# Optimization experiments

Measured on AMD Instinct MI355X. Metric: run time of the kernel, lower is better.

The kernel has to match this reference:

```python
import math
import jax, jax.numpy as jnp
import numpy as np

D_MODEL, N_HEADS, D_HEAD, D_INNER = 512, 8, 64, 2048
QLEN, MLEN, BATCH = 2048, 2048, 2


def _layernorm(x, g, b, eps=1e-5):
    mu = jnp.mean(x, axis=-1, keepdims=True)
    var = jnp.var(x, axis=-1, keepdims=True)
    return (x - mu) * jax.lax.rsqrt(var + eps) * g + b


def _rel_shift(x):
    # x: [qlen, klen, B, n] -> Transformer-XL relative shift
    q, k, b, n = x.shape
    x = jnp.pad(x, ((0, 0), (1, 0), (0, 0), (0, 0)))  # zero-pad key dim at front
    x = x.reshape(k + 1, q, b, n)[1:].reshape(q, k, b, n)
    return x


def setup_inputs() -> dict:
    key = jax.random.key(0)
    ks = jax.random.split(key, 16)
    nd = N_HEADS * D_HEAD
    s = 0.02
    return {
        "x": jax.random.normal(ks[0], (QLEN, BATCH, D_MODEL), jnp.float32),
        "r": jax.random.normal(ks[1], (QLEN + MLEN, D_MODEL), jnp.float32),
        "u": jax.random.normal(ks[2], (N_HEADS, D_HEAD), jnp.float32) * s,
        "v": jax.random.normal(ks[3], (N_HEADS, D_HEAD), jnp.float32) * s,
        "mems": jax.random.normal(ks[4], (MLEN, BATCH, D_MODEL), jnp.float32),
        "Wqkv": jax.random.normal(ks[5], (3 * nd, D_MODEL), jnp.float32) * s,
        "Wr": jax.random.normal(ks[6], (nd, D_MODEL), jnp.float32) * s,
        "Wo": jax.random.normal(ks[7], (D_MODEL, nd), jnp.float32) * s,
        "ln1_g": jnp.ones((D_MODEL,), jnp.float32),
        "ln1_b": jnp.zeros((D_MODEL,), jnp.float32),
        "W1": jax.random.normal(ks[8], (D_MODEL, D_INNER), jnp.float32) * s,
        "b1": jnp.zeros((D_INNER,), jnp.float32),
        "W2": jax.random.normal(ks[9], (D_INNER, D_MODEL), jnp.float32) * s,
        "b2": jnp.zeros((D_MODEL,), jnp.float32),
        "ln2_g": jnp.ones((D_MODEL,), jnp.float32),
        "ln2_b": jnp.zeros((D_MODEL,), jnp.float32),
    }


def reference(x, r, u, v, mems, Wqkv, Wr, Wo, ln1_g, ln1_b, W1, b1, W2, b2, ln2_g, ln2_b):
    qlen, B, d_model = x.shape
    n_heads, d_head = u.shape
    cat = jnp.concatenate([mems, x], axis=0)          # [klen, B, d_model]
    klen = cat.shape[0]
    mlen = klen - qlen

    qkv = cat @ Wqkv.T                                 # [klen, B, 3*n*d]
    q, k, val = jnp.split(qkv, 3, axis=-1)
    q = q[-qlen:].reshape(qlen, B, n_heads, d_head)
    k = k.reshape(klen, B, n_heads, d_head)
    val = val.reshape(klen, B, n_heads, d_head)
    rk = (r @ Wr.T).reshape(klen, n_heads, d_head)     # relative key heads

    AC = jnp.einsum('ibnd,jbnd->ijbn', q + u, k)       # content score
    BD = _rel_shift(jnp.einsum('ibnd,jnd->ijbn', q + v, rk))  # position score
    score = (AC + BD) * (1.0 / math.sqrt(d_head))      # [qlen, klen, B, n]

    # causal mask with memory: query i attends keys j <= i + mlen
    mask = jnp.arange(klen)[None, :] > (jnp.arange(qlen)[:, None] + mlen)
    score = jnp.where(mask[:, :, None, None], jnp.float32(-1e30), score)
    attn = jax.nn.softmax(score, axis=1)

    out = jnp.einsum('ijbn,jbnd->ibnd', attn, val).reshape(qlen, B, n_heads * d_head)
    out = out @ Wo.T
    h = _layernorm(x + out, ln1_g, ln1_b)              # post-LN attention

    core = jax.nn.relu(h @ W1 + b1) @ W2 + b2          # PositionwiseFF
    return _layernorm(h + core, ln2_g, ln2_b)
```

## Files before the change

### kernel.cpp

```cpp
#include <hip/hip_runtime.h>
#include <hip/hip_bf16.h>

#define QLEN 2048
#define MLEN 2048
#define KLEN 4096
#define BATCH 2
#define DMODEL 512
#define NHEADS 8
#define DHEAD 64
#define DINNER 2048

typedef __attribute__((ext_vector_type(8))) short  vs8;
typedef __attribute__((ext_vector_type(8))) __bf16 vbf8;
typedef __attribute__((ext_vector_type(4))) float  vf4;

__device__ __forceinline__ float bf2f(ushort h) {
    union { unsigned u; float f; } c; c.u = ((unsigned)h) << 16; return c.f;
}
__device__ __forceinline__ ushort f2bf(float f) {
    return __builtin_bit_cast(unsigned short, (__bf16)f);
}
__device__ __forceinline__ vf4 mfma16(vs8 a, vs8 b, vf4 c) {
    return __builtin_amdgcn_mfma_f32_16x16x32_bf16(
        __builtin_bit_cast(vbf8, a), __builtin_bit_cast(vbf8, b), c, 0, 0, 0);
}
__device__ __forceinline__ void gl16(const ushort* g, ushort* l) {
    __builtin_amdgcn_global_load_lds(
        (const __attribute__((address_space(1))) void*)g,
        (__attribute__((address_space(3))) void*)l, 16, 0, 0);
}
#define WAITV4 asm volatile("s_waitcnt vmcnt(4)" ::: "memory")
#define WAITV0 asm volatile("s_waitcnt vmcnt(0)" ::: "memory")
__device__ __forceinline__ void barx() {
    asm volatile("" ::: "memory");
    __builtin_amdgcn_s_barrier();
    asm volatile("" ::: "memory");
}

__global__ void cvt_bf(const float* __restrict__ in, ushort* __restrict__ out, int nel4) {
    int i = blockIdx.x * 256 + threadIdx.x;
    if (i < nel4) {
        float4 f = ((const float4*)in)[i];
        ushort4 o; o.x = f2bf(f.x); o.y = f2bf(f.y); o.z = f2bf(f.z); o.w = f2bf(f.w);
        ((ushort4*)out)[i] = o;
    }
}

__global__ void cvt_cat(const float* __restrict__ mems, const float* __restrict__ x,
                        ushort* __restrict__ out) {
    int i = blockIdx.x * 256 + threadIdx.x;
    const int half4 = MLEN * BATCH * DMODEL / 4;
    if (i < 2 * half4) {
        float4 f = (i < half4) ? ((const float4*)mems)[i] : ((const float4*)x)[i - half4];
        ushort4 o; o.x = f2bf(f.x); o.y = f2bf(f.y); o.z = f2bf(f.z); o.w = f2bf(f.w);
        ((ushort4*)out)[i] = o;
    }
}

__global__ void cvt_tr(const float* __restrict__ in, ushort* __restrict__ out, int R, int C) {
    __shared__ float t[32][33];
    const int c0 = blockIdx.x * 32, r0 = blockIdx.y * 32;
    const int tx = threadIdx.x & 31, ty = threadIdx.x >> 5;
#pragma unroll
    for (int q = 0; q < 4; ++q) {
        int r = ty + q * 8;
        t[r][tx] = in[(size_t)(r0 + r) * C + c0 + tx];
    }
    __syncthreads();
#pragma unroll
    for (int q = 0; q < 4; ++q) {
        int c = ty + q * 8;
        out[(size_t)(c0 + c) * R + r0 + tx] = f2bf(t[tx][c]);
    }
}

__global__ void vtrans(const ushort* __restrict__ qkv, ushort* __restrict__ vT) {
    __shared__ __align__(16) ushort t_lds[64][72];
    const int j0 = blockIdx.x * 64, n = blockIdx.y, b = blockIdx.z;
    const int tid = threadIdx.x;
#pragma unroll
    for (int p = 0; p < 2; ++p) {
        int u2 = p * 256 + tid;
        int j = u2 >> 3, d8 = (u2 & 7) * 8;
        vs8 v8 = *(const vs8*)(qkv + ((size_t)(j0 + j) * BATCH + b) * 1536 + 1024 + n * 64 + d8);
#pragma unroll
        for (int e = 0; e < 8; ++e) t_lds[d8 + e][j] = (ushort)v8[e];
    }
    __syncthreads();
#pragma unroll
    for (int p = 0; p < 2; ++p) {
        int u2 = p * 256 + tid;
        int d = u2 >> 3, j8 = (u2 & 7) * 8;
        vs8 o8 = *(const vs8*)&t_lds[d][j8];
        *(vs8*)(vT + ((size_t)(b * NHEADS + n) * 64 + d) * KLEN + j0 + j8) = o8;
    }
}

template <int EPI>
__global__ __launch_bounds__(256)
void gemm_bt(const ushort* __restrict__ A, const ushort* __restrict__ B,
             void* __restrict__ C0, void* __restrict__ C1,
             const float* __restrict__ bias, int M, int N, int K, int kc, int ldc) {
    __shared__ __align__(16) ushort As[2][128 * 32];
    __shared__ __align__(16) ushort Bs[2][128 * 32];
    const int n0 = blockIdx.x * 128;
    const int m0 = blockIdx.y * 128;
    const int kb = blockIdx.z * kc;
    void* C = blockIdx.z ? C1 : C0;
    const int tid = threadIdx.x;
    const int lane = tid & 63, wave = tid >> 6;
    const int wr = wave >> 1, wc = wave & 1;
    const int lr = lane & 15, lg = lane >> 4;
    vf4 acc[4][4] = {};

    auto stage = [&](int bi, int k0) {
#pragma unroll
        for (int t = 0; t < 2; ++t) {
            int u = t * 256 + tid;
            int row = u >> 2, cu = u & 3;
            int sc = cu ^ ((row >> 1) & 3);
            gl16(&A[(size_t)(m0 + row) * K + k0 + sc * 8],
                 &As[bi][t * 2048 + (tid & 192) * 8]);
            gl16(&B[(size_t)(n0 + row) * K + k0 + sc * 8],
                 &Bs[bi][t * 2048 + (tid & 192) * 8]);
        }
    };

    const int nt = kc >> 5;
    stage(0, kb);
    int cur = 0;
    for (int t = 0; t < nt; ++t) {
        if (t + 1 < nt) { stage(cur ^ 1, kb + (t + 1) * 32); WAITV4; }
        else { WAITV0; }
        barx();
        vs8 af[4], bfr[4];
#pragma unroll
        for (int m = 0; m < 4; ++m) {
            int rr = wr * 64 + m * 16 + lr;
            af[m] = *(const vs8*)&As[cur][rr * 32 + (lg ^ ((rr >> 1) & 3)) * 8];
        }
#pragma unroll
        for (int nn = 0; nn < 4; ++nn) {
            int rr = wc * 64 + nn * 16 + lr;
            bfr[nn] = *(const vs8*)&Bs[cur][rr * 32 + (lg ^ ((rr >> 1) & 3)) * 8];
        }
#pragma unroll
        for (int m = 0; m < 4; ++m)
#pragma unroll
            for (int nn = 0; nn < 4; ++nn)
                acc[m][nn] = mfma16(af[m], bfr[nn], acc[m][nn]);
        barx();
        cur ^= 1;
    }

#pragma unroll
    for (int m = 0; m < 4; ++m) {
#pragma unroll
        for (int nn = 0; nn < 4; ++nn) {
            int row0 = m0 + wr * 64 + m * 16 + lg * 4;
            int col  = n0 + wc * 64 + nn * 16 + lr;
#pragma unroll
            for (int rr = 0; rr < 4; ++rr) {
                float vv = acc[m][nn][rr];
                size_t off = (size_t)(row0 + rr) * ldc + col;
                if (EPI == 0) ((float*)C)[off] = vv;
                else if (EPI == 1) ((ushort*)C)[off] = f2bf(vv);
                else if (EPI == 2) {
                    float t2 = vv + bias[col];
                    ((ushort*)C)[off] = f2bf(t2 > 0.f ? t2 : 0.f);
                } else {
                    ((ushort*)C)[(((size_t)(col >> 6)) << 18) + (size_t)(row0 + rr) * 64 + (col & 63)]
                        = f2bf(vv);
                }
            }
        }
    }
}

__global__ __launch_bounds__(256, 3)
void attn2(const ushort* __restrict__ qkv, const ushort* __restrict__ rkh,
           const ushort* __restrict__ vT, const float* __restrict__ uu,
           const float* __restrict__ vv, float* __restrict__ part_l,
           float* __restrict__ part_o) {
    __shared__ __align__(16) ushort K_lds[64 * 64];
    __shared__ __align__(16) ushort V_lds[64 * 64];
    __shared__ __align__(16) ushort w_lds[4][16 * 84];
    __shared__ __align__(16) ushort p_lds[4][16 * 72];

    const int chunk = blockIdx.x & 3, qb = 31 - (blockIdx.x >> 2);
    const int b = blockIdx.y, n = blockIdx.z;
    const int tid = threadIdx.x, lane = tid & 63, w = tid >> 6;
    const int lr = lane & 15, lg = lane >> 4;
    const int i0w = qb * 64 + w * 16;

    ushort* wl = w_lds[w];
    ushort* pl = p_lds[w];
    const ushort* rh  = rkh + ((size_t)n << 18);
    const ushort* vTh = vT + (size_t)(b * NHEADS + n) * 64 * KLEN;

    const float S = 0.18033688011112042f;
    vs8 aqu[2], aqv[2];
#pragma unroll
    for (int kk = 0; kk < 2; ++kk) {
        int d0 = kk * 32 + lg * 8;
        vs8 q8 = *(const vs8*)(qkv + ((size_t)(i0w + lr + MLEN) * BATCH + b) * 1536 + n * 64 + d0);
#pragma unroll
        for (int e = 0; e < 8; ++e) {
            float qf = bf2f((ushort)q8[e]);
            aqu[kk][e] = (short)f2bf((qf + uu[n * 64 + d0 + e]) * S);
            aqv[kk][e] = (short)f2bf((qf + vv[n * 64 + d0 + e]) * S);
        }
    }

    const vf4 zero4 = {0.f, 0.f, 0.f, 0.f};
    vf4 o[4] = {zero4, zero4, zero4, zero4};
    float l_run[4] = {0.f, 0.f, 0.f, 0.f};

    const int jstart = chunk * 1024;
    int avail = qb * 64 + 2111 - jstart;
    int niter = avail < 0 ? 0 : (avail >> 6) + 1;
    niter = niter > 16 ? 16 : niter;

    const int slot = lane & 7;
    vs8 kreg[2], vreg[2];
    auto ldkv = [&](int j0) {
#pragma unroll
        for (int p2 = 0; p2 < 2; ++p2) {
            int row = p2 * 32 + w * 8 + (lane >> 3);
            int g = (slot - row) & 7;
            kreg[p2] = *(const vs8*)(qkv + ((size_t)(j0 + row) * BATCH + b) * 1536 + 512 + n * 64 + g * 8);
            vreg[p2] = *(const vs8*)(vTh + (size_t)row * KLEN + j0 + g * 8);
        }
    };
    auto wrkv = [&]() {
#pragma unroll
        for (int p2 = 0; p2 < 2; ++p2) {
            int row = p2 * 32 + w * 8 + (lane >> 3);
            *(vs8*)&K_lds[row * 64 + slot * 8] = kreg[p2];
            *(vs8*)&V_lds[row * 64 + slot * 8] = vreg[p2];
        }
    };

    if (niter > 0) {
        ldkv(jstart);
        wrkv();
        __syncthreads();
        for (int it = 0; it < niter; ++it) {
            const int j0 = jstart + it * 64;
            const bool more = (it + 1 < niter);
            if (more) ldkv(j0 + 64);

            vf4 acc_s[4] = {zero4, zero4, zero4, zero4};
#pragma unroll
            for (int q = 0; q < 4; ++q) {
                int jr = q * 16 + lr;
#pragma unroll
                for (int kk = 0; kk < 2; ++kk) {
                    vs8 kb = *(const vs8*)&K_lds[jr * 64 + ((kk * 4 + lg + jr) & 7) * 8];
                    acc_s[q] = mfma16(aqu[kk], kb, acc_s[q]);
                }
            }
            const int mbase = j0 - i0w + 2032;
#pragma unroll
            for (int wg = 0; wg < 5; ++wg) {
                vf4 aw = zero4;
                int mrow = mbase + wg * 16 + lr;
                mrow = mrow > KLEN - 1 ? KLEN - 1 : mrow;
#pragma unroll
                for (int kk = 0; kk < 2; ++kk) {
                    vs8 rb = *(const vs8*)(rh + (size_t)mrow * 64 + kk * 32 + lg * 8);
                    aw = mfma16(aqv[kk], rb, aw);
                }
#pragma unroll
                for (int r = 0; r < 4; ++r)
                    wl[(lg * 4 + r) * 84 + wg * 16 + lr] = f2bf(aw[r]);
            }

            const int thr = qb * 64 + w * 16 + 2048 - j0;
            if (thr >= 63) {
#pragma unroll
                for (int r = 0; r < 4; ++r) {
                    int il = lg * 4 + r;
                    float psum = 0.f;
#pragma unroll
                    for (int q = 0; q < 4; ++q) {
                        int jl = q * 16 + lr;
                        float p4 = __builtin_amdgcn_exp2f(
                            acc_s[q][r] + bf2f(wl[il * 84 + jl - il + 15]));
                        psum += p4;
                        pl[il * 72 + jl] = f2bf(p4);
                    }
#pragma unroll
                    for (int off = 1; off < 16; off <<= 1) psum += __shfl_xor(psum, off);
                    l_run[r] += psum;
                }
            } else {
#pragma unroll
                for (int r = 0; r < 4; ++r) {
                    int il = lg * 4 + r;
                    float psum = 0.f;
#pragma unroll
                    for (int q = 0; q < 4; ++q) {
                        int jl = q * 16 + lr;
                        float s = acc_s[q][r] + bf2f(wl[il * 84 + jl - il + 15]);
                        if (jl - il > thr) s = -1e30f;
                        float p4 = __builtin_amdgcn_exp2f(s);
                        psum += p4;
                        pl[il * 72 + jl] = f2bf(p4);
                    }
#pragma unroll
                    for (int off = 1; off < 16; off <<= 1) psum += __shfl_xor(psum, off);
                    l_run[r] += psum;
                }
            }

#pragma unroll
            for (int jk = 0; jk < 2; ++jk) {
                vs8 pf = *(const vs8*)&pl[lr * 72 + jk * 32 + lg * 8];
#pragma unroll
                for (int dg = 0; dg < 4; ++dg) {
                    int dr = dg * 16 + lr;
                    vs8 vfr = *(const vs8*)&V_lds[dr * 64 + ((jk * 4 + lg + dr) & 7) * 8];
                    o[dg] = mfma16(pf, vfr, o[dg]);
                }
            }
            __syncthreads();
            if (more) { wrkv(); __syncthreads(); }
        }
    }

#pragma unroll
    for (int r = 0; r < 4; ++r) {
        int i = i0w + lg * 4 + r;
        int pr = (i * 2 + b) * 8 + n;
        size_t base = ((size_t)chunk * 32768 + pr) * 64;
#pragma unroll
        for (int dg = 0; dg < 4; ++dg)
            part_o[base + dg * 16 + lr] = o[dg][r];
        if (lr == 0) part_l[chunk * 32768 + pr] = l_run[r];
    }
}

__global__ __launch_bounds__(256)
void combine(const float* __restrict__ part_l, const float* __restrict__ part_o,
             ushort* __restrict__ ao) {
    int t = blockIdx.x * 256 + threadIdx.x;
    int pr = t >> 4, d4 = (t & 15) * 4;
    float l = 0.f;
    float4 s = {0.f, 0.f, 0.f, 0.f};
#pragma unroll
    for (int c = 0; c < 4; ++c) {
        l += part_l[c * 32768 + pr];
        float4 a = *(const float4*)&part_o[((size_t)c * 32768 + pr) * 64 + d4];
        s.x += a.x; s.y += a.y; s.z += a.z; s.w += a.w;
    }
    float rl = 1.f / l;
    int i2b = pr >> 3, n = pr & 7;
    ushort* dst = ao + (size_t)i2b * 512 + n * 64 + d4;
    dst[0] = f2bf(s.x * rl);
    dst[1] = f2bf(s.y * rl);
    dst[2] = f2bf(s.z * rl);
    dst[3] = f2bf(s.w * rl);
}

__global__ __launch_bounds__(256)
void ln_fuse(const float* __restrict__ base, const float* __restrict__ pa,
             const float* __restrict__ pb, const float* __restrict__ bias,
             const float* __restrict__ g, const float* __restrict__ bb,
             float* __restrict__ of32, ushort* __restrict__ obf) {
    const int row = blockIdx.x * 4 + (threadIdx.x >> 6);
    const int lane = threadIdx.x & 63;
    const size_t off0 = (size_t)row * DMODEL + lane * 8;
    float vals[8];
    float s = 0.f, s2 = 0.f;
#pragma unroll
    for (int e = 0; e < 8; ++e) {
        float t = base[off0 + e] + pa[off0 + e];
        if (pb) t += pb[off0 + e];
        if (bias) t += bias[lane * 8 + e];
        vals[e] = t; s += t; s2 += t * t;
    }
#pragma unroll
    for (int o = 1; o < 64; o <<= 1) { s += __shfl_xor(s, o); s2 += __shfl_xor(s2, o); }
    const float mean = s * (1.f / DMODEL);
    const float var = s2 * (1.f / DMODEL) - mean * mean;
    const float rstd = rsqrtf(var + 1e-5f);
#pragma unroll
    for (int e = 0; e < 8; ++e) {
        int c = lane * 8 + e;
        float y = (vals[e] - mean) * rstd * g[c] + bb[c];
        if (of32) of32[(size_t)row * DMODEL + c] = y;
        if (obf)  obf[(size_t)row * DMODEL + c] = f2bf(y);
    }
}

extern "C" void kernel_launch(void* const* d_in, const int* in_sizes, int n_in,
                              void* d_out, int out_size, void* d_ws, size_t ws_size,
                              hipStream_t stream) {
    const float* x    = (const float*)d_in[0];
    const float* r    = (const float*)d_in[1];
    const float* u    = (const float*)d_in[2];
    const float* v    = (const float*)d_in[3];
    const float* mems = (const float*)d_in[4];
    const float* Wqkv = (const float*)d_in[5];
    const float* Wr   = (const float*)d_in[6];
    const float* Wo   = (const float*)d_in[7];
    const float* ln1g = (const float*)d_in[8];
    const float* ln1b = (const float*)d_in[9];
    const float* W1   = (const float*)d_in[10];
    const float* b1   = (const float*)d_in[11];
    const float* W2   = (const float*)d_in[12];
    const float* b2   = (const float*)d_in[13];
    const float* ln2g = (const float*)d_in[14];
    const float* ln2b = (const float*)d_in[15];
    float* out = (float*)d_out;

    char* p = (char*)d_ws;
    auto alloc = [&](size_t bytes) { char* q = p; p += (bytes + 255) & ~(size_t)255; return q; };
    const size_t MB84 = (size_t)QLEN * BATCH * 512 * 4;
    ushort* cat_bf  = (ushort*)alloc((size_t)KLEN * BATCH * DMODEL * 2);
    ushort* wqkv_bf = (ushort*)alloc((size_t)1536 * 512 * 2);
    ushort* r_bf    = (ushort*)alloc((size_t)KLEN * 512 * 2);
    ushort* wr_bf   = (ushort*)alloc((size_t)512 * 512 * 2);
    ushort* wo_bf   = (ushort*)alloc((size_t)512 * 512 * 2);
    ushort* w1t_bf  = (ushort*)alloc((size_t)DINNER * 512 * 2);
    ushort* w2t_bf  = (ushort*)alloc((size_t)512 * DINNER * 2);
    ushort* qkv_bf  = (ushort*)alloc((size_t)KLEN * BATCH * 1536 * 2);
    ushort* rkh_bf  = (ushort*)alloc((size_t)KLEN * 512 * 2);
    ushort* vT      = (ushort*)alloc((size_t)BATCH * NHEADS * 64 * KLEN * 2);
    ushort* ao_bf   = (ushort*)alloc((size_t)QLEN * BATCH * 512 * 2);
    ushort* h_bf    = (ushort*)alloc((size_t)QLEN * BATCH * 512 * 2);
    float*  part_l  = (float*)alloc((size_t)4 * 32768 * 4);
    char*   big     = alloc(5 * MB84);
    float*  part_o  = (float*)big;
    float*  proj1a  = (float*)big;
    float*  proj1b  = (float*)(big + MB84);
    float*  h_f32   = (float*)(big + 2 * MB84);
    ushort* ff1_bf  = (ushort*)(big + 3 * MB84);
    float*  proj2a  = proj1a;
    float*  proj2b  = proj1b;

    const int MROWS = QLEN * BATCH;
    const int CATROWS = KLEN * BATCH;

    cvt_cat<<<(CATROWS * DMODEL / 4 + 255) / 256, 256, 0, stream>>>(mems, x, cat_bf);
    cvt_bf<<<(KLEN * 512 / 4 + 255) / 256, 256, 0, stream>>>(r, r_bf, KLEN * 512 / 4);
    cvt_bf<<<(1536 * 512 / 4 + 255) / 256, 256, 0, stream>>>(Wqkv, wqkv_bf, 1536 * 512 / 4);
    cvt_bf<<<(512 * 512 / 4 + 255) / 256, 256, 0, stream>>>(Wr, wr_bf, 512 * 512 / 4);
    cvt_bf<<<(512 * 512 / 4 + 255) / 256, 256, 0, stream>>>(Wo, wo_bf, 512 * 512 / 4);
    cvt_tr<<<dim3(DINNER / 32, 512 / 32), 256, 0, stream>>>(W1, w1t_bf, 512, DINNER);
    cvt_tr<<<dim3(512 / 32, DINNER / 32), 256, 0, stream>>>(W2, w2t_bf, DINNER, 512);

    gemm_bt<1><<<dim3(1024 / 128, CATROWS / 128, 1), 256, 0, stream>>>(
        cat_bf, wqkv_bf + (size_t)512 * 512, qkv_bf + 512, nullptr, nullptr,
        CATROWS, 1024, 512, 512, 1536);
    gemm_bt<1><<<dim3(512 / 128, 4096 / 128, 1), 256, 0, stream>>>(
        cat_bf + (size_t)4096 * 512, wqkv_bf, qkv_bf + (size_t)4096 * 1536, nullptr, nullptr,
        4096, 512, 512, 512, 1536);
    gemm_bt<3><<<dim3(512 / 128, KLEN / 128, 1), 256, 0, stream>>>(
        r_bf, wr_bf, rkh_bf, nullptr, nullptr, KLEN, 512, 512, 512, 512);

    vtrans<<<dim3(KLEN / 64, NHEADS, BATCH), 256, 0, stream>>>(qkv_bf, vT);
    attn2<<<dim3(128, BATCH, NHEADS), 256, 0, stream>>>(qkv_bf, rkh_bf, vT, u, v, part_l, part_o);
    combine<<<32768 * 16 / 256, 256, 0, stream>>>(part_l, part_o, ao_bf);

    gemm_bt<0><<<dim3(512 / 128, MROWS / 128, 2), 256, 0, stream>>>(
        ao_bf, wo_bf, proj1a, proj1b, nullptr, MROWS, 512, 512, 256, 512);
    ln_fuse<<<MROWS / 4, 256, 0, stream>>>(x, proj1a, proj1b, nullptr, ln1g, ln1b, h_f32, h_bf);

    gemm_bt<2><<<dim3(DINNER / 128, MROWS / 128, 1), 256, 0, stream>>>(
        h_bf, w1t_bf, ff1_bf, nullptr, b1, MROWS, DINNER, 512, 512, 2048);
    gemm_bt<0><<<dim3(512 / 128, MROWS / 128, 2), 256, 0, stream>>>(
        ff1_bf, w2t_bf, proj2a, proj2b, nullptr, MROWS, 512, 2048, 1024, 512);
    ln_fuse<<<MROWS / 4, 256, 0, stream>>>(h_f32, proj2a, proj2b, b2, ln2g, ln2b, out, nullptr);
}
```

Measured before the change: 356.5 us.

## Transpose attention MFMAs to keep P in registers, halve key-split chunks

The attention kernel now computes scores transposed (K as the A operand), so the probability tile stays in registers. It is packed to bf16 and redistributed with lane shuffles instead of being staged through per-wave LDS. The key range is split into 2 chunks instead of 4, and the partial outputs are written as bf16 via a coalesced LDS staging step. This shrinks the combine pass and the partial-result traffic. Occupancy hint rises to 5 waves per SIMD, at the cost of fewer blocks, longer per-block loops and bf16 rounding of the partial sums.

```diff
diff --git a/kernel.cpp b/kernel.cpp
--- a/kernel.cpp
+++ b/kernel.cpp
@@ -19,6 +19,11 @@
 }
 __device__ __forceinline__ ushort f2bf(float f) {
     return __builtin_bit_cast(unsigned short, (__bf16)f);
+}
+__device__ __forceinline__ unsigned cvtpk(float lo, float hi) {
+    unsigned r;
+    asm("v_cvt_pk_bf16_f32 %0, %1, %2" : "=v"(r) : "v"(lo), "v"(hi));
+    return r;
 }
 __device__ __forceinline__ vf4 mfma16(vs8 a, vs8 b, vf4 c) {
     return __builtin_amdgcn_mfma_f32_16x16x32_bf16(
@@ -177,24 +182,22 @@
     }
 }
 
-__global__ __launch_bounds__(256, 3)
+__global__ __launch_bounds__(256, 5)
 void attn2(const ushort* __restrict__ qkv, const ushort* __restrict__ rkh,
            const ushort* __restrict__ vT, const float* __restrict__ uu,
            const float* __restrict__ vv, float* __restrict__ part_l,
-           float* __restrict__ part_o) {
+           ushort* __restrict__ part_o) {
     __shared__ __align__(16) ushort K_lds[64 * 64];
     __shared__ __align__(16) ushort V_lds[64 * 64];
     __shared__ __align__(16) ushort w_lds[4][16 * 84];
-    __shared__ __align__(16) ushort p_lds[4][16 * 72];
-
-    const int chunk = blockIdx.x & 3, qb = 31 - (blockIdx.x >> 2);
+
+    const int chunk = blockIdx.x & 1, qb = 31 - (blockIdx.x >> 1);
     const int b = blockIdx.y, n = blockIdx.z;
     const int tid = threadIdx.x, lane = tid & 63, w = tid >> 6;
     const int lr = lane & 15, lg = lane >> 4;
     const int i0w = qb * 64 + w * 16;
 
     ushort* wl = w_lds[w];
-    ushort* pl = p_lds[w];
     const ushort* rh  = rkh + ((size_t)n << 18);
     const ushort* vTh = vT + (size_t)(b * NHEADS + n) * 64 * KLEN;
 
@@ -214,12 +217,12 @@
 
     const vf4 zero4 = {0.f, 0.f, 0.f, 0.f};
     vf4 o[4] = {zero4, zero4, zero4, zero4};
-    float l_run[4] = {0.f, 0.f, 0.f, 0.f};
-
-    const int jstart = chunk * 1024;
+    float l_run = 0.f;
+
+    const int jstart = chunk * 2048;
     int avail = qb * 64 + 2111 - jstart;
     int niter = avail < 0 ? 0 : (avail >> 6) + 1;
-    niter = niter > 16 ? 16 : niter;
+    niter = niter > 32 ? 32 : niter;
 
     const int slot = lane & 7;
     vs8 kreg[2], vreg[2];
@@ -241,126 +244,128 @@
         }
     };
 
-    if (niter > 0) {
-        ldkv(jstart);
-        wrkv();
+    ldkv(jstart);
+    wrkv();
+    __syncthreads();
+    for (int it = 0; it < niter; ++it) {
+        const int j0 = jstart + it * 64;
+        const bool more = (it + 1 < niter);
+        if (more) ldkv(j0 + 64);
+
+        vf4 acc_s[4] = {zero4, zero4, zero4, zero4};
+#pragma unroll
+        for (int jg = 0; jg < 4; ++jg) {
+            int jr = jg * 16 + lr;
+#pragma unroll
+            for (int kk = 0; kk < 2; ++kk) {
+                vs8 kb = *(const vs8*)&K_lds[jr * 64 + ((kk * 4 + lg + jr) & 7) * 8];
+                acc_s[jg] = mfma16(kb, aqu[kk], acc_s[jg]);
+            }
+        }
+        const int mbase = j0 - i0w + 2032;
+#pragma unroll
+        for (int wg = 0; wg < 5; ++wg) {
+            vf4 aw = zero4;
+            int mrow = mbase + wg * 16 + lr;
+            mrow = mrow > KLEN - 1 ? KLEN - 1 : mrow;
+#pragma unroll
+            for (int kk = 0; kk < 2; ++kk) {
+                vs8 rb = *(const vs8*)(rh + (size_t)mrow * 64 + kk * 32 + lg * 8);
+                aw = mfma16(rb, aqv[kk], aw);
+            }
+#pragma unroll
+            for (int r = 0; r < 4; ++r)
+                wl[lr * 84 + wg * 16 + lg * 4 + r] = f2bf(aw[r]);
+        }
+
+        const int thr = i0w + 2048 - j0;
+        const int bw = lr * 83 + 15;
+        if (thr >= 63) {
+#pragma unroll
+            for (int jg = 0; jg < 4; ++jg)
+#pragma unroll
+                for (int r = 0; r < 4; ++r) {
+                    float p4 = __builtin_amdgcn_exp2f(
+                        acc_s[jg][r] + bf2f(wl[bw + jg * 16 + lg * 4 + r]));
+                    acc_s[jg][r] = p4;
+                    l_run += p4;
+                }
+        } else {
+#pragma unroll
+            for (int jg = 0; jg < 4; ++jg)
+#pragma unroll
+                for (int r = 0; r < 4; ++r) {
+                    int jrel = jg * 16 + lg * 4 + r;
+                    float p4 = (jrel - lr > thr) ? 0.f
+                        : __builtin_amdgcn_exp2f(
+                              acc_s[jg][r] + bf2f(wl[bw + jg * 16 + lg * 4 + r]));
+                    acc_s[jg][r] = p4;
+                    l_run += p4;
+                }
+        }
+
+        unsigned pw0[4], pw1[4];
+#pragma unroll
+        for (int jg = 0; jg < 4; ++jg) {
+            pw0[jg] = cvtpk(acc_s[jg][0], acc_s[jg][1]);
+            pw1[jg] = cvtpk(acc_s[jg][2], acc_s[jg][3]);
+        }
+
+        const int srcA = (lg & 1) * 32 + lr, srcB = srcA + 16;
+        const bool hi = (lg >> 1) != 0;
+#pragma unroll
+        for (int kk = 0; kk < 2; ++kk) {
+            unsigned a0 = __shfl(pw0[2 * kk], srcA), b0 = __shfl(pw0[2 * kk + 1], srcA);
+            unsigned a1 = __shfl(pw1[2 * kk], srcA), b1 = __shfl(pw1[2 * kk + 1], srcA);
+            unsigned a2 = __shfl(pw0[2 * kk], srcB), b2 = __shfl(pw0[2 * kk + 1], srcB);
+            unsigned a3 = __shfl(pw1[2 * kk], srcB), b3 = __shfl(pw1[2 * kk + 1], srcB);
+            int4 pu = { (int)(hi ? b0 : a0), (int)(hi ? b1 : a1),
+                        (int)(hi ? b2 : a2), (int)(hi ? b3 : a3) };
+            vs8 pfrag = __builtin_bit_cast(vs8, pu);
+#pragma unroll
+            for (int dg = 0; dg < 4; ++dg) {
+                int dr = dg * 16 + lr;
+                vs8 vfr = *(const vs8*)&V_lds[dr * 64 + ((kk * 4 + lg + dr) & 7) * 8];
+                o[dg] = mfma16(vfr, pfrag, o[dg]);
+            }
+        }
         __syncthreads();
-        for (int it = 0; it < niter; ++it) {
-            const int j0 = jstart + it * 64;
-            const bool more = (it + 1 < niter);
-            if (more) ldkv(j0 + 64);
-
-            vf4 acc_s[4] = {zero4, zero4, zero4, zero4};
-#pragma unroll
-            for (int q = 0; q < 4; ++q) {
-                int jr = q * 16 + lr;
-#pragma unroll
-                for (int kk = 0; kk < 2; ++kk) {
-                    vs8 kb = *(const vs8*)&K_lds[jr * 64 + ((kk * 4 + lg + jr) & 7) * 8];
-                    acc_s[q] = mfma16(aqu[kk], kb, acc_s[q]);
-                }
-            }
-            const int mbase = j0 - i0w + 2032;
-#pragma unroll
-            for (int wg = 0; wg < 5; ++wg) {
-                vf4 aw = zero4;
-                int mrow = mbase + wg * 16 + lr;
-                mrow = mrow > KLEN - 1 ? KLEN - 1 : mrow;
-#pragma unroll
-                for (int kk = 0; kk < 2; ++kk) {
-                    vs8 rb = *(const vs8*)(rh + (size_t)mrow * 64 + kk * 32 + lg * 8);
-                    aw = mfma16(aqv[kk], rb, aw);
-                }
-#pragma unroll
-                for (int r = 0; r < 4; ++r)
-                    wl[(lg * 4 + r) * 84 + wg * 16 + lr] = f2bf(aw[r]);
-            }
-
-            const int thr = qb * 64 + w * 16 + 2048 - j0;
-            if (thr >= 63) {
-#pragma unroll
-                for (int r = 0; r < 4; ++r) {
-                    int il = lg * 4 + r;
-                    float psum = 0.f;
-#pragma unroll
-                    for (int q = 0; q < 4; ++q) {
-                        int jl = q * 16 + lr;
-                        float p4 = __builtin_amdgcn_exp2f(
-                            acc_s[q][r] + bf2f(wl[il * 84 + jl - il + 15]));
-                        psum += p4;
-                        pl[il * 72 + jl] = f2bf(p4);
-                    }
-#pragma unroll
-                    for (int off = 1; off < 16; off <<= 1) psum += __shfl_xor(psum, off);
-                    l_run[r] += psum;
-                }
-            } else {
-#pragma unroll
-                for (int r = 0; r < 4; ++r) {
-                    int il = lg * 4 + r;
-                    float psum = 0.f;
-#pragma unroll
-                    for (int q = 0; q < 4; ++q) {
-                        int jl = q * 16 + lr;
-                        float s = acc_s[q][r] + bf2f(wl[il * 84 + jl - il + 15]);
-                        if (jl - il > thr) s = -1e30f;
-                        float p4 = __builtin_amdgcn_exp2f(s);
-                        psum += p4;
-                        pl[il * 72 + jl] = f2bf(p4);
-                    }
-#pragma unroll
-                    for (int off = 1; off < 16; off <<= 1) psum += __shfl_xor(psum, off);
-                    l_run[r] += psum;
-                }
-            }
-
-#pragma unroll
-            for (int jk = 0; jk < 2; ++jk) {
-                vs8 pf = *(const vs8*)&pl[lr * 72 + jk * 32 + lg * 8];
-#pragma unroll
-                for (int dg = 0; dg < 4; ++dg) {
-                    int dr = dg * 16 + lr;
-                    vs8 vfr = *(const vs8*)&V_lds[dr * 64 + ((jk * 4 + lg + dr) & 7) * 8];
-                    o[dg] = mfma16(pf, vfr, o[dg]);
-                }
-            }
-            __syncthreads();
-            if (more) { wrkv(); __syncthreads(); }
-        }
-    }
-
-#pragma unroll
-    for (int r = 0; r < 4; ++r) {
-        int i = i0w + lg * 4 + r;
-        int pr = (i * 2 + b) * 8 + n;
-        size_t base = ((size_t)chunk * 32768 + pr) * 64;
-#pragma unroll
-        for (int dg = 0; dg < 4; ++dg)
-            part_o[base + dg * 16 + lr] = o[dg][r];
-        if (lr == 0) part_l[chunk * 32768 + pr] = l_run[r];
-    }
+        if (more) { wrkv(); __syncthreads(); }
+    }
+
+    float l1 = l_run + __shfl_xor(l_run, 16);
+    float l_tot = l1 + __shfl_xor(l1, 32);
+
+#pragma unroll
+    for (int dg = 0; dg < 4; ++dg) {
+        uint2 uu2 = { cvtpk(o[dg][0], o[dg][1]), cvtpk(o[dg][2], o[dg][3]) };
+        *(uint2*)&wl[lr * 68 + dg * 16 + lg * 4] = uu2;
+    }
+    const int q2 = lane >> 2, dp = (lane & 3) * 16;
+    const int i2 = i0w + q2;
+    size_t gbase = ((size_t)chunk * 32768 + ((size_t)(i2 * 2 + b) * 8 + n)) * 64 + dp;
+    vs8 r0 = *(const vs8*)&wl[q2 * 68 + dp];
+    vs8 r1 = *(const vs8*)&wl[q2 * 68 + dp + 8];
+    *(vs8*)&part_o[gbase] = r0;
+    *(vs8*)&part_o[gbase + 8] = r1;
+    if (lg == 0)
+        part_l[chunk * 32768 + ((i0w + lr) * 2 + b) * 8 + n] = l_tot;
 }
 
 __global__ __launch_bounds__(256)
-void combine(const float* __restrict__ part_l, const float* __restrict__ part_o,
+void combine(const float* __restrict__ part_l, const ushort* __restrict__ part_o,
              ushort* __restrict__ ao) {
     int t = blockIdx.x * 256 + threadIdx.x;
-    int pr = t >> 4, d4 = (t & 15) * 4;
-    float l = 0.f;
-    float4 s = {0.f, 0.f, 0.f, 0.f};
-#pragma unroll
-    for (int c = 0; c < 4; ++c) {
-        l += part_l[c * 32768 + pr];
-        float4 a = *(const float4*)&part_o[((size_t)c * 32768 + pr) * 64 + d4];
-        s.x += a.x; s.y += a.y; s.z += a.z; s.w += a.w;
-    }
-    float rl = 1.f / l;
+    int pr = t >> 3, d8 = (t & 7) * 8;
+    float rl = 1.f / (part_l[pr] + part_l[32768 + pr]);
+    vs8 a = *(const vs8*)&part_o[(size_t)pr * 64 + d8];
+    vs8 c = *(const vs8*)&part_o[(size_t)(32768 + pr) * 64 + d8];
+    vs8 ov;
+#pragma unroll
+    for (int e = 0; e < 8; ++e)
+        ov[e] = (short)f2bf((bf2f((ushort)a[e]) + bf2f((ushort)c[e])) * rl);
     int i2b = pr >> 3, n = pr & 7;
-    ushort* dst = ao + (size_t)i2b * 512 + n * 64 + d4;
-    dst[0] = f2bf(s.x * rl);
-    dst[1] = f2bf(s.y * rl);
-    dst[2] = f2bf(s.z * rl);
-    dst[3] = f2bf(s.w * rl);
+    *(vs8*)(ao + (size_t)i2b * 512 + n * 64 + d8) = ov;
 }
 
 __global__ __launch_bounds__(256)
@@ -430,9 +435,9 @@
     ushort* vT      = (ushort*)alloc((size_t)BATCH * NHEADS * 64 * KLEN * 2);
     ushort* ao_bf   = (ushort*)alloc((size_t)QLEN * BATCH * 512 * 2);
     ushort* h_bf    = (ushort*)alloc((size_t)QLEN * BATCH * 512 * 2);
-    float*  part_l  = (float*)alloc((size_t)4 * 32768 * 4);
+    float*  part_l  = (float*)alloc((size_t)2 * 32768 * 4);
     char*   big     = alloc(5 * MB84);
-    float*  part_o  = (float*)big;
+    ushort* part_o  = (ushort*)big;
     float*  proj1a  = (float*)big;
     float*  proj1b  = (float*)(big + MB84);
     float*  h_f32   = (float*)(big + 2 * MB84);
@@ -461,8 +466,8 @@
         r_bf, wr_bf, rkh_bf, nullptr, nullptr, KLEN, 512, 512, 512, 512);
 
     vtrans<<<dim3(KLEN / 64, NHEADS, BATCH), 256, 0, stream>>>(qkv_bf, vT);
-    attn2<<<dim3(128, BATCH, NHEADS), 256, 0, stream>>>(qkv_bf, rkh_bf, vT, u, v, part_l, part_o);
-    combine<<<32768 * 16 / 256, 256, 0, stream>>>(part_l, part_o, ao_bf);
+    attn2<<<dim3(64, BATCH, NHEADS), 256, 0, stream>>>(qkv_bf, rkh_bf, vT, u, v, part_l, part_o);
+    combine<<<32768 * 8 / 256, 256, 0, stream>>>(part_l, part_o, ao_bf);
 
     gemm_bt<0><<<dim3(512 / 128, MROWS / 128, 2), 256, 0, stream>>>(
         ao_bf, wo_bf, proj1a, proj1b, nullptr, MROWS, 512, 512, 256, 512);
```

Measured after the change: 454.7 us. 27.5% more time.
